# Kernel optimization log

Hardware: AMD Instinct MI355X
Metric: run time of the kernel (lower is better)

## Reference

```python
import jax, jax.numpy as jnp
import numpy as np

DIM = 512
NUM_HEADS = 8


def setup_inputs() -> dict:
    key = jax.random.key(0)
    k1, k2, k3, k4, k5 = jax.random.split(key, 5)
    B, N, C = 4, 4096, DIM
    x = jax.random.normal(k1, (B, N, C), dtype=jnp.float32)
    # Conv1d kernel_size=1 weights, squeezed to [out, in]
    qkv_w = jax.random.normal(k2, (3 * C, C), dtype=jnp.float32) * (C ** -0.5)
    qkv_b = jax.random.normal(k3, (3 * C,), dtype=jnp.float32) * 0.02
    out_w = jax.random.normal(k4, (C, C), dtype=jnp.float32) * (C ** -0.5)
    out_b = jax.random.normal(k5, (C,), dtype=jnp.float32) * 0.02
    return {"x": x, "qkv_w": qkv_w, "qkv_b": qkv_b, "out_w": out_w, "out_b": out_b}


def reference(x, qkv_w, qkv_b, out_w, out_b):
    B, N, C = x.shape
    H = NUM_HEADS
    hd = C // H
    scale = hd ** -0.5
    # 1x1 Conv1d == per-position linear: [B,N,C] x [3C,C] -> [B,N,3C]
    qkv = jnp.einsum('bnc,oc->bno', x, qkv_w) + qkv_b
    qkv = qkv.reshape(B, N, 3, H, hd)
    q, k, v = qkv[:, :, 0], qkv[:, :, 1], qkv[:, :, 2]  # each [B,N,H,hd]
    # NOTE: faithful to the original: q @ k.transpose(-2,-1) contracts head_dim
    # giving an [B,N,H,H] score matrix (attention across heads per position).
    scores = jnp.einsum('bnhd,bngd->bnhg', q, k) * scale
    attn = jax.nn.softmax(scores, axis=-1)
    out = jnp.einsum('bnhg,bngd->bnhd', attn, v)  # [B,N,H,hd]
    # Faithful to original: transpose(1,2) then reshape(B,N,C) interleaves axes.
    out = out.transpose(0, 2, 1, 3).reshape(B, N, C)
    out = jnp.einsum('bnc,oc->bno', out, out_w) + out_b
    return out
```

## Files before the change

### kernel.cpp

```cpp
#include <hip/hip_runtime.h>
#include <hip/hip_bf16.h>

#define DIMC 512
#define SEQ 4096
#define M_TOK 16384
#define N_QKV 1536

typedef __bf16 bfv8 __attribute__((ext_vector_type(8)));
typedef float f32v4 __attribute__((ext_vector_type(4)));
typedef unsigned short u16v8 __attribute__((ext_vector_type(8)));

static __device__ __forceinline__ float bf2f(unsigned short u) {
    union { unsigned int i; float f; } x; x.i = ((unsigned int)u) << 16; return x.f;
}
static __device__ __forceinline__ unsigned short f2bf(float f) {
    union { float f; unsigned int i; } x; x.f = f;
    unsigned int r = x.i + 0x7FFFu + ((x.i >> 16) & 1u);
    return (unsigned short)(r >> 16);
}

static __device__ __forceinline__ void gload_lds16(const void* g, void* s) {
    __builtin_amdgcn_global_load_lds(
        (const __attribute__((address_space(1))) unsigned int*)g,
        (__attribute__((address_space(3))) unsigned int*)s, 16, 0, 0);
}

#define NX8  (M_TOK * DIMC / 8)
#define NWQ8 (N_QKV * DIMC / 8)
#define NWO8 (DIMC * DIMC / 8)
__global__ __launch_bounds__(256) void cvt_all(
    const float* __restrict__ x,  const float* __restrict__ wq,
    const float* __restrict__ wo, unsigned short* __restrict__ xb,
    unsigned short* __restrict__ wqb, unsigned short* __restrict__ wob)
{
    int i = blockIdx.x * 256 + threadIdx.x;
    const float* src; unsigned short* dst; int off;
    if (i < NX8)             { src = x;  dst = xb;  off = i; }
    else if (i < NX8 + NWQ8) { src = wq; dst = wqb; off = i - NX8; }
    else                     { src = wo; dst = wob; off = i - NX8 - NWQ8; }
    const float4* p = (const float4*)src + (size_t)off * 2;
    float4 a = p[0], b = p[1];
    u16v8 o;
    o[0] = f2bf(a.x); o[1] = f2bf(a.y); o[2] = f2bf(a.z); o[3] = f2bf(a.w);
    o[4] = f2bf(b.x); o[5] = f2bf(b.y); o[6] = f2bf(b.z); o[7] = f2bf(b.w);
    *(u16v8*)(dst + (size_t)off * 8) = o;
}

template<bool OUT_BF16>
__global__ __launch_bounds__(256) void gemm_nt_bk64(
    const unsigned short* __restrict__ A,
    const unsigned short* __restrict__ B,
    const float* __restrict__ bias,
    void* __restrict__ Cout,
    int M, int N, int K)
{
    __shared__ __align__(16) unsigned short As[128 * 64];
    __shared__ __align__(16) unsigned short Bs[128 * 64];
    const int tid  = threadIdx.x;
    const int lane = tid & 63;
    const int wid  = tid >> 6;
    const int wm   = wid >> 1;
    const int wn   = wid & 1;
    const int m0 = blockIdx.x * 128;
    const int n0 = blockIdx.y * 128;
    const int frow = lane & 15;
    const int fcol = (lane >> 4) * 8;

    f32v4 acc[4][4] = {};

    const unsigned short* aSrc[4];
    const unsigned short* bSrc[4];
    #pragma unroll
    for (int s = 0; s < 4; ++s) {
        int p = s * 2048 + tid * 8;
        int row = p >> 6;
        int col = (p ^ (((p >> 6) & 7) << 3)) & 63;
        aSrc[s] = A + (size_t)(m0 + row) * K + col;
        bSrc[s] = B + (size_t)(n0 + row) * K + col;
    }
    unsigned short* aDst = As + (tid >> 6) * 512;
    unsigned short* bDst = Bs + (tid >> 6) * 512;

    for (int kt = 0; kt < (K >> 6); ++kt) {
        #pragma unroll
        for (int s = 0; s < 4; ++s) {
            gload_lds16(aSrc[s] + kt * 64, aDst + s * 2048);
            gload_lds16(bSrc[s] + kt * 64, bDst + s * 2048);
        }
        __syncthreads();
        #pragma unroll
        for (int ks = 0; ks < 2; ++ks) {
            bfv8 af[4], bf[4];
            #pragma unroll
            for (int i = 0; i < 4; ++i) {
                const int r = wm * 64 + i * 16 + frow;
                const int e = r * 64 + ks * 32 + fcol;
                af[i] = *(const bfv8*)(As + (e ^ ((r & 7) << 3)));
            }
            #pragma unroll
            for (int j = 0; j < 4; ++j) {
                const int r = wn * 64 + j * 16 + frow;
                const int e = r * 64 + ks * 32 + fcol;
                bf[j] = *(const bfv8*)(Bs + (e ^ ((r & 7) << 3)));
            }
            #pragma unroll
            for (int i = 0; i < 4; ++i)
                #pragma unroll
                for (int j = 0; j < 4; ++j)
                    acc[i][j] = __builtin_amdgcn_mfma_f32_16x16x32_bf16(
                        af[i], bf[j], acc[i][j], 0, 0, 0);
        }
        __syncthreads();
    }

    const int erow = (lane >> 4) * 4;
    const int ecol = lane & 15;
    #pragma unroll
    for (int j = 0; j < 4; ++j) {
        const int col = n0 + wn * 64 + j * 16 + ecol;
        const float bv = bias[col];
        #pragma unroll
        for (int i = 0; i < 4; ++i) {
            const int rbase = m0 + wm * 64 + i * 16 + erow;
            #pragma unroll
            for (int r = 0; r < 4; ++r) {
                const float v = acc[i][j][r] + bv;
                if constexpr (OUT_BF16)
                    ((unsigned short*)Cout)[(size_t)(rbase + r) * N + col] = f2bf(v);
                else
                    ((float*)Cout)[(size_t)(rbase + r) * N + col] = v;
            }
        }
    }
}

__global__ __launch_bounds__(256) void attn_mix2(
    const unsigned short* __restrict__ Y1,
    unsigned short* __restrict__ Y2)
{
    const int tid  = threadIdx.x;
    const int tok  = blockIdx.x * 16 + (tid >> 4);
    const int l16  = tid & 15;
    const int h    = l16 >> 1;
    const int half = l16 & 1;
    const unsigned short* qkv = Y1 + (size_t)tok * N_QKV;

    float qf[32];
    #pragma unroll
    for (int c = 0; c < 4; ++c) {
        u16v8 v = *(const u16v8*)(qkv + h * 64 + half * 32 + c * 8);
        #pragma unroll
        for (int j = 0; j < 8; ++j) qf[c * 8 + j] = bf2f(v[j]);
    }
    float sc[8];
    #pragma unroll
    for (int g = 0; g < 8; ++g) {
        const unsigned short* kp = qkv + DIMC + g * 64 + half * 32;
        float a = 0.f;
        #pragma unroll
        for (int c = 0; c < 4; ++c) {
            u16v8 v = *(const u16v8*)(kp + c * 8);
            #pragma unroll
            for (int j = 0; j < 8; ++j) a = fmaf(qf[c * 8 + j], bf2f(v[j]), a);
        }
        a += __shfl_xor(a, 1);
        sc[g] = a * 0.125f;
    }
    float mx = sc[0];
    #pragma unroll
    for (int g = 1; g < 8; ++g) mx = fmaxf(mx, sc[g]);
    float sum = 0.f;
    #pragma unroll
    for (int g = 0; g < 8; ++g) { sc[g] = __expf(sc[g] - mx); sum += sc[g]; }
    const float inv = 1.f / sum;
    #pragma unroll
    for (int g = 0; g < 8; ++g) sc[g] *= inv;

    float o[32] = {};
    #pragma unroll
    for (int g = 0; g < 8; ++g) {
        const unsigned short* vp = qkv + 2 * DIMC + g * 64 + half * 32;
        #pragma unroll
        for (int c = 0; c < 4; ++c) {
            u16v8 v = *(const u16v8*)(vp + c * 8);
            #pragma unroll
            for (int j = 0; j < 8; ++j) o[c * 8 + j] = fmaf(sc[g], bf2f(v[j]), o[c * 8 + j]);
        }
    }
    const int n = tok & (SEQ - 1);
    const int b = tok >> 12;
    const size_t drow = (size_t)b * SEQ + h * 512 + (n >> 3);
    unsigned short* dst = Y2 + drow * DIMC + ((n & 7) << 6) + half * 32;
    #pragma unroll
    for (int c = 0; c < 4; ++c) {
        u16v8 ov;
        #pragma unroll
        for (int j = 0; j < 8; ++j) ov[j] = f2bf(o[c * 8 + j]);
        *(u16v8*)(dst + c * 8) = ov;
    }
}

extern "C" void kernel_launch(void* const* d_in, const int* in_sizes, int n_in,
                              void* d_out, int out_size, void* d_ws, size_t ws_size,
                              hipStream_t stream) {
    const float* x     = (const float*)d_in[0];
    const float* qkv_w = (const float*)d_in[1];
    const float* qkv_b = (const float*)d_in[2];
    const float* out_w = (const float*)d_in[3];
    const float* out_b = (const float*)d_in[4];
    float* out = (float*)d_out;

    unsigned short* Y1 = (unsigned short*)d_ws;
    unsigned short* Xb = Y1 + (size_t)M_TOK * N_QKV;
    unsigned short* Y2 = Xb;
    unsigned short* Wq = Xb + (size_t)M_TOK * DIMC;
    unsigned short* Wo = Wq + (size_t)N_QKV * DIMC;

    cvt_all<<<(NX8 + NWQ8 + NWO8) / 256, 256, 0, stream>>>(x, qkv_w, out_w, Xb, Wq, Wo);

    gemm_nt_bk64<true><<<dim3(M_TOK / 128, N_QKV / 128), 256, 0, stream>>>(
        Xb, Wq, qkv_b, Y1, M_TOK, N_QKV, DIMC);

    attn_mix2<<<M_TOK / 16, 256, 0, stream>>>(Y1, Y2);

    gemm_nt_bk64<false><<<dim3(M_TOK / 128, DIMC / 128), 256, 0, stream>>>(
        Y2, Wo, out_b, out, M_TOK, DIMC, DIMC);
}
```

Before: 85.72 us.

## Double-buffer GEMM LDS tiles with BK=32 to overlap loads and MFMA

Both GEMMs now use two ping-pong LDS buffers with K-tile 32 instead of one 64-wide buffer. The next tile's global-to-LDS loads are issued before computing on the current tile, and each iteration needs one barrier instead of two. The LDS swizzle is reworked for the 32-element row stride. The aim is to hide global load latency behind MFMA work. The cost is twice as many loop iterations, each with less work to amortise the barrier over.

After: 83.98 us. 1.02x faster.

```diff
diff --git a/kernel.cpp b/kernel.cpp
--- a/kernel.cpp
+++ b/kernel.cpp
@@ -47,15 +47,15 @@
 }
 
 template<bool OUT_BF16>
-__global__ __launch_bounds__(256) void gemm_nt_bk64(
+__global__ __launch_bounds__(256) void gemm_nt_2ph(
     const unsigned short* __restrict__ A,
     const unsigned short* __restrict__ B,
     const float* __restrict__ bias,
     void* __restrict__ Cout,
     int M, int N, int K)
 {
-    __shared__ __align__(16) unsigned short As[128 * 64];
-    __shared__ __align__(16) unsigned short Bs[128 * 64];
+    __shared__ __align__(16) unsigned short As[2][128 * 32];
+    __shared__ __align__(16) unsigned short Bs[2][128 * 32];
     const int tid  = threadIdx.x;
     const int lane = tid & 63;
     const int wid  = tid >> 6;
@@ -65,53 +65,56 @@
     const int n0 = blockIdx.y * 128;
     const int frow = lane & 15;
     const int fcol = (lane >> 4) * 8;
+    const int NT = K >> 5;
 
     f32v4 acc[4][4] = {};
 
-    const unsigned short* aSrc[4];
-    const unsigned short* bSrc[4];
-    #pragma unroll
-    for (int s = 0; s < 4; ++s) {
-        int p = s * 2048 + tid * 8;
-        int row = p >> 6;
-        int col = (p ^ (((p >> 6) & 7) << 3)) & 63;
+    const unsigned short* aSrc[2];
+    const unsigned short* bSrc[2];
+    #pragma unroll
+    for (int s = 0; s < 2; ++s) {
+        const int p   = (s * 256 + tid) * 8;
+        const int row = p >> 5;
+        const int col = (p & 31) ^ (((row >> 1) & 3) << 3);
         aSrc[s] = A + (size_t)(m0 + row) * K + col;
         bSrc[s] = B + (size_t)(n0 + row) * K + col;
     }
-    unsigned short* aDst = As + (tid >> 6) * 512;
-    unsigned short* bDst = Bs + (tid >> 6) * 512;
-
-    for (int kt = 0; kt < (K >> 6); ++kt) {
-        #pragma unroll
-        for (int s = 0; s < 4; ++s) {
-            gload_lds16(aSrc[s] + kt * 64, aDst + s * 2048);
-            gload_lds16(bSrc[s] + kt * 64, bDst + s * 2048);
-        }
+    const int dstOff[2] = { wid * 512, 2048 + wid * 512 };
+
+#define STAGE(kt, buf)                                                         \
+    {                                                                          \
+        _Pragma("unroll") for (int s = 0; s < 2; ++s) {                        \
+            gload_lds16(aSrc[s] + (kt) * 32, &As[buf][dstOff[s]]);             \
+            gload_lds16(bSrc[s] + (kt) * 32, &Bs[buf][dstOff[s]]);             \
+        }                                                                      \
+    }
+
+    STAGE(0, 0)
+    __syncthreads();
+
+    for (int t = 0; t < NT; ++t) {
+        const int p = t & 1;
+        if (t + 1 < NT) STAGE(t + 1, p ^ 1)
+        bfv8 af[4], bf[4];
+        #pragma unroll
+        for (int i = 0; i < 4; ++i) {
+            const int r = wm * 64 + i * 16 + frow;
+            af[i] = *(const bfv8*)(&As[p][r * 32 + (fcol ^ (((r >> 1) & 3) << 3))]);
+        }
+        #pragma unroll
+        for (int j = 0; j < 4; ++j) {
+            const int r = wn * 64 + j * 16 + frow;
+            bf[j] = *(const bfv8*)(&Bs[p][r * 32 + (fcol ^ (((r >> 1) & 3) << 3))]);
+        }
+        #pragma unroll
+        for (int i = 0; i < 4; ++i)
+            #pragma unroll
+            for (int j = 0; j < 4; ++j)
+                acc[i][j] = __builtin_amdgcn_mfma_f32_16x16x32_bf16(
+                    af[i], bf[j], acc[i][j], 0, 0, 0);
         __syncthreads();
-        #pragma unroll
-        for (int ks = 0; ks < 2; ++ks) {
-            bfv8 af[4], bf[4];
-            #pragma unroll
-            for (int i = 0; i < 4; ++i) {
-                const int r = wm * 64 + i * 16 + frow;
-                const int e = r * 64 + ks * 32 + fcol;
-                af[i] = *(const bfv8*)(As + (e ^ ((r & 7) << 3)));
-            }
-            #pragma unroll
-            for (int j = 0; j < 4; ++j) {
-                const int r = wn * 64 + j * 16 + frow;
-                const int e = r * 64 + ks * 32 + fcol;
-                bf[j] = *(const bfv8*)(Bs + (e ^ ((r & 7) << 3)));
-            }
-            #pragma unroll
-            for (int i = 0; i < 4; ++i)
-                #pragma unroll
-                for (int j = 0; j < 4; ++j)
-                    acc[i][j] = __builtin_amdgcn_mfma_f32_16x16x32_bf16(
-                        af[i], bf[j], acc[i][j], 0, 0, 0);
-        }
-        __syncthreads();
-    }
+    }
+#undef STAGE
 
     const int erow = (lane >> 4) * 4;
     const int ecol = lane & 15;
@@ -218,11 +221,11 @@
 
     cvt_all<<<(NX8 + NWQ8 + NWO8) / 256, 256, 0, stream>>>(x, qkv_w, out_w, Xb, Wq, Wo);
 
-    gemm_nt_bk64<true><<<dim3(M_TOK / 128, N_QKV / 128), 256, 0, stream>>>(
+    gemm_nt_2ph<true><<<dim3(M_TOK / 128, N_QKV / 128), 256, 0, stream>>>(
         Xb, Wq, qkv_b, Y1, M_TOK, N_QKV, DIMC);
 
     attn_mix2<<<M_TOK / 16, 256, 0, stream>>>(Y1, Y2);
 
-    gemm_nt_bk64<false><<<dim3(M_TOK / 128, DIMC / 128), 256, 0, stream>>>(
+    gemm_nt_2ph<false><<<dim3(M_TOK / 128, DIMC / 128), 256, 0, stream>>>(
         Y2, Wo, out_b, out, M_TOK, DIMC, DIMC);
 }
```
